# Optimization experiments

Hardware: AMD Instinct MI355X
Metric: run time of the kernel (lower is better)

The kernel has to match this reference:

```python
import jax, jax.numpy as jnp
import numpy as np

B, S, V, K = 8, 128, 32000, 32


def setup_inputs() -> dict:
    key = jax.random.key(0)
    ks = jax.random.split(key, 8)
    return {
        "neural_logit": jax.random.normal(ks[0], (B, S, V), dtype=jnp.float32),
        "optor_vals": jax.random.randint(ks[1], (B, S, K), 0, V),
        "optor_dists": jax.random.uniform(ks[2], (B, S, K), dtype=jnp.float32) * 100.0,
        "const_vals": jax.random.randint(ks[3], (B, S, K), 0, V),
        "const_dists": jax.random.uniform(ks[4], (B, S, K), dtype=jnp.float32) * 100.0,
        "prev_words": jax.random.randint(ks[5], (B, S), 0, V),
        "optor_lamda": jnp.array([0.7], dtype=jnp.float32),
        "const_lamda": jnp.array([0.7], dtype=jnp.float32),
        "optor_temp": jnp.array([10.0], dtype=jnp.float32),
        "const_temp": jnp.array([10.0], dtype=jnp.float32),
    }


def _knn_prob(vals, dists, temp, vocab):
    # kernel-density: softmax over negative distances, scatter-add into vocab ids
    b, s, k = vals.shape
    w = jax.nn.softmax(-dists / temp, axis=-1)            # [B,S,K]
    rows = jnp.arange(b * s)[:, None]                     # [BS,1]
    p = jnp.zeros((b * s, vocab), w.dtype)
    p = p.at[rows, vals.reshape(b * s, k)].add(w.reshape(b * s, k))
    return p.reshape(b, s, vocab)


def reference(neural_logit, optor_vals, optor_dists, const_vals, const_dists,
              prev_words, optor_lamda, const_lamda, optor_temp, const_temp):
    nmt_prob = jax.nn.softmax(neural_logit, axis=-1)      # [B,S,V]

    optor_knn = _knn_prob(optor_vals, optor_dists, optor_temp[0], V)
    optor_combined = optor_lamda[0] * optor_knn + (1.0 - optor_lamda[0]) * nmt_prob

    const_knn = _knn_prob(const_vals, const_dists, const_temp[0], V)
    const_combined = const_lamda[0] * const_knn + (1.0 - const_lamda[0]) * nmt_prob

    pw = prev_words                                        # [B,S]
    optor_mask = (pw <= 88) | ((pw >= 91) & (pw <= 291))
    const_mask = (pw == 89) | (pw == 90) | (pw >= 292)

    combined = (optor_combined * optor_mask[:, :, None].astype(nmt_prob.dtype)
                + const_combined * const_mask[:, :, None].astype(nmt_prob.dtype))
    return combined
```

## Files before the change

### kernel.cpp

```cpp
#include <hip/hip_runtime.h>
#include <math.h>

constexpr int Bc = 8, Sc = 128, Vc = 32000, Kc = 32;
constexpr int NROWS = Bc * Sc;
constexpr int V4 = Vc / 4;
constexpr int NT = 256;
constexpr int ITF = V4 / NT;
constexpr int TAIL = V4 - ITF * NT;
constexpr int NW = NT / 64;

typedef float vfloat4 __attribute__((ext_vector_type(4)));

__global__ __launch_bounds__(NT) void SR_knnModel_kernel(
    const float* __restrict__ logit,
    const int*   __restrict__ optor_vals,
    const float* __restrict__ optor_dists,
    const int*   __restrict__ const_vals,
    const float* __restrict__ const_dists,
    const int*   __restrict__ prev_words,
    const float* __restrict__ optor_lamda,
    const float* __restrict__ const_lamda,
    const float* __restrict__ optor_temp,
    const float* __restrict__ const_temp,
    float* __restrict__ out)
{
    const int row = blockIdx.x;
    const int t   = threadIdx.x;
    const size_t base = (size_t)row * Vc;
    const float4* __restrict__ xin  = (const float4*)(logit + base);
    float* __restrict__        orow = out + base;

    float lsum = 0.f;
#pragma unroll 4
    for (int i = 0; i < ITF; ++i) {
        const float4 v = xin[t + i * NT];
        lsum += (__expf(v.x) + __expf(v.y)) + (__expf(v.z) + __expf(v.w));
    }
    if (t < TAIL) {
        const float4 v = xin[ITF * NT + t];
        lsum += (__expf(v.x) + __expf(v.y)) + (__expf(v.z) + __expf(v.w));
    }

    const int pw = prev_words[row];
    const float ol = optor_lamda[0];
    const float cl = const_lamda[0];

#pragma unroll
    for (int off = 32; off > 0; off >>= 1)
        lsum += __shfl_xor(lsum, off);
    __shared__ float red[NW];
    if ((t & 63) == 0) red[t >> 6] = lsum;
    __syncthreads();
    float S = red[0];
#pragma unroll
    for (int w = 1; w < NW; ++w) S += red[w];

    const bool om_ = (pw <= 88) || (pw >= 91 && pw <= 291);
    const bool cm_ = (pw == 89) || (pw == 90) || (pw >= 292);
    const float omf = om_ ? 1.f : 0.f;
    const float cmf = cm_ ? 1.f : 0.f;
    const float cn = (1.f - ol) * omf + (1.f - cl) * cmf;
    const float f = cn / S;

#pragma unroll 4
    for (int i = 0; i < ITF; ++i) {
        const int idx = t + i * NT;
        const float4 v = xin[idx];
        vfloat4 o;
        o.x = __expf(v.x) * f;
        o.y = __expf(v.y) * f;
        o.z = __expf(v.z) * f;
        o.w = __expf(v.w) * f;
        __builtin_nontemporal_store(o, (vfloat4*)orow + idx);
    }
    if (t < TAIL) {
        const int idx = ITF * NT + t;
        const float4 v = xin[idx];
        vfloat4 o;
        o.x = __expf(v.x) * f;
        o.y = __expf(v.y) * f;
        o.z = __expf(v.z) * f;
        o.w = __expf(v.w) * f;
        __builtin_nontemporal_store(o, (vfloat4*)orow + idx);
    }
    __syncthreads();

    if (t < 32 || (t >= 64 && t < 96)) {
        const bool is_opt = (t < 32);
        const float scale = is_opt ? ol * omf : cl * cmf;
        if (scale != 0.f) {
            const int k = t & 31;
            const int*   vals  = is_opt ? optor_vals  : const_vals;
            const float* dists = is_opt ? optor_dists : const_dists;
            const float  temp  = is_opt ? optor_temp[0] : const_temp[0];
            const float sc = -dists[row * Kc + k] / temp;
            float mm = sc;
#pragma unroll
            for (int off = 16; off > 0; off >>= 1)
                mm = fmaxf(mm, __shfl_xor(mm, off));
            const float e = __expf(sc - mm);
            float sm = e;
#pragma unroll
            for (int off = 16; off > 0; off >>= 1)
                sm += __shfl_xor(sm, off);
            const float w = e / sm;
            atomicAdd(out + base + vals[row * Kc + k], scale * w);
        }
    }
}

extern "C" void kernel_launch(void* const* d_in, const int* in_sizes, int n_in,
                              void* d_out, int out_size, void* d_ws, size_t ws_size,
                              hipStream_t stream) {
    const float* logit       = (const float*)d_in[0];
    const int*   optor_vals  = (const int*)  d_in[1];
    const float* optor_dists = (const float*)d_in[2];
    const int*   const_vals  = (const int*)  d_in[3];
    const float* const_dists = (const float*)d_in[4];
    const int*   prev_words  = (const int*)  d_in[5];
    const float* optor_lamda = (const float*)d_in[6];
    const float* const_lamda = (const float*)d_in[7];
    const float* optor_temp  = (const float*)d_in[8];
    const float* const_temp  = (const float*)d_in[9];
    float* out = (float*)d_out;

    SR_knnModel_kernel<<<NROWS, NT, 0, stream>>>(
        logit, optor_vals, optor_dists, const_vals, const_dists, prev_words,
        optor_lamda, const_lamda, optor_temp, const_temp, out);
}
```

Measured before the change: 264.1 us.

## Split fused softmax kernel into sum, chunked scale, and scatter kernels

The single per-row kernel is replaced by three launches: one computes each row's exp-sum into workspace, a second writes the scaled probabilities with four blocks per row, and a third does the kNN scatter-add with one wave per row. The aim is more parallelism in the write pass and removing the block-wide syncs. The cost is two extra launches and a second read of the logits from memory or cache, where the fused version reread its own row.

```diff
diff --git a/kernel.cpp b/kernel.cpp
--- a/kernel.cpp
+++ b/kernel.cpp
@@ -4,15 +4,105 @@
 constexpr int Bc = 8, Sc = 128, Vc = 32000, Kc = 32;
 constexpr int NROWS = Bc * Sc;
 constexpr int V4 = Vc / 4;
-constexpr int NT = 256;
-constexpr int ITF = V4 / NT;
-constexpr int TAIL = V4 - ITF * NT;
-constexpr int NW = NT / 64;
+
+constexpr int NTA = 256;
+constexpr int ITA = V4 / NTA;
+constexpr int TLA = V4 - ITA * NTA;
+constexpr int NWA = NTA / 64;
+
+constexpr int CHUNKS = 4;
+constexpr int C4 = V4 / CHUNKS;
+constexpr int NTB = 256;
+constexpr int ITB = C4 / NTB;
+constexpr int TLB = C4 - ITB * NTB;
+
+constexpr int NTC = 256;
+constexpr int RPC = 4;
 
 typedef float vfloat4 __attribute__((ext_vector_type(4)));
 
-__global__ __launch_bounds__(NT) void SR_knnModel_kernel(
+
+__global__ __launch_bounds__(NTA) void SR_knn_sum(
     const float* __restrict__ logit,
+    float* __restrict__ ws)
+{
+    const int row = blockIdx.x;
+    const int t   = threadIdx.x;
+    const float4* __restrict__ xin = (const float4*)(logit + (size_t)row * Vc);
+
+    float lsum = 0.f;
+#pragma unroll 4
+    for (int i = 0; i < ITA; ++i) {
+        const float4 v = xin[t + i * NTA];
+        lsum += (__expf(v.x) + __expf(v.y)) + (__expf(v.z) + __expf(v.w));
+    }
+    if (t < TLA) {
+        const float4 v = xin[ITA * NTA + t];
+        lsum += (__expf(v.x) + __expf(v.y)) + (__expf(v.z) + __expf(v.w));
+    }
+
+#pragma unroll
+    for (int off = 32; off > 0; off >>= 1)
+        lsum += __shfl_xor(lsum, off);
+    __shared__ float red[NWA];
+    if ((t & 63) == 0) red[t >> 6] = lsum;
+    __syncthreads();
+    if (t == 0) {
+        float S = red[0];
+#pragma unroll
+        for (int w = 1; w < NWA; ++w) S += red[w];
+        ws[row] = S;
+    }
+}
+
+__global__ __launch_bounds__(NTB) void SR_knn_scale(
+    const float* __restrict__ logit,
+    const float* __restrict__ ws,
+    const int*   __restrict__ prev_words,
+    const float* __restrict__ optor_lamda,
+    const float* __restrict__ const_lamda,
+    float* __restrict__ out)
+{
+    const int g   = blockIdx.x;
+    const int row = g >> 2;
+    const int c   = g & (CHUNKS - 1);
+    const int t   = threadIdx.x;
+    const size_t base = (size_t)row * Vc;
+    const int off4 = c * C4;
+    const float4* __restrict__ xin  = (const float4*)(logit + base) + off4;
+    vfloat4* __restrict__      xout = (vfloat4*)(out + base) + off4;
+
+    const int pw = prev_words[row];
+    const bool om_ = (pw <= 88) || (pw >= 91 && pw <= 291);
+    const bool cm_ = (pw == 89) || (pw == 90) || (pw >= 292);
+    const float cn = (1.f - optor_lamda[0]) * (om_ ? 1.f : 0.f)
+                   + (1.f - const_lamda[0]) * (cm_ ? 1.f : 0.f);
+    const float f = cn / ws[row];
+
+#pragma unroll
+    for (int i = 0; i < ITB; ++i) {
+        const int idx = t + i * NTB;
+        const float4 v = xin[idx];
+        vfloat4 o;
+        o.x = __expf(v.x) * f;
+        o.y = __expf(v.y) * f;
+        o.z = __expf(v.z) * f;
+        o.w = __expf(v.w) * f;
+        __builtin_nontemporal_store(o, xout + idx);
+    }
+    if (t < TLB) {
+        const int idx = ITB * NTB + t;
+        const float4 v = xin[idx];
+        vfloat4 o;
+        o.x = __expf(v.x) * f;
+        o.y = __expf(v.y) * f;
+        o.z = __expf(v.z) * f;
+        o.w = __expf(v.w) * f;
+        __builtin_nontemporal_store(o, xout + idx);
+    }
+}
+
+__global__ __launch_bounds__(NTC) void SR_knn_scatter(
     const int*   __restrict__ optor_vals,
     const float* __restrict__ optor_dists,
     const int*   __restrict__ const_vals,
@@ -24,88 +114,34 @@
     const float* __restrict__ const_temp,
     float* __restrict__ out)
 {
-    const int row = blockIdx.x;
-    const int t   = threadIdx.x;
-    const size_t base = (size_t)row * Vc;
-    const float4* __restrict__ xin  = (const float4*)(logit + base);
-    float* __restrict__        orow = out + base;
-
-    float lsum = 0.f;
-#pragma unroll 4
-    for (int i = 0; i < ITF; ++i) {
-        const float4 v = xin[t + i * NT];
-        lsum += (__expf(v.x) + __expf(v.y)) + (__expf(v.z) + __expf(v.w));
-    }
-    if (t < TAIL) {
-        const float4 v = xin[ITF * NT + t];
-        lsum += (__expf(v.x) + __expf(v.y)) + (__expf(v.z) + __expf(v.w));
-    }
+    const int t    = threadIdx.x;
+    const int wave = t >> 6;
+    const int row  = blockIdx.x * RPC + wave;
+    const int lane = t & 63;
+    const bool is_opt = lane < 32;
+    const int k = lane & 31;
 
     const int pw = prev_words[row];
-    const float ol = optor_lamda[0];
-    const float cl = const_lamda[0];
-
-#pragma unroll
-    for (int off = 32; off > 0; off >>= 1)
-        lsum += __shfl_xor(lsum, off);
-    __shared__ float red[NW];
-    if ((t & 63) == 0) red[t >> 6] = lsum;
-    __syncthreads();
-    float S = red[0];
-#pragma unroll
-    for (int w = 1; w < NW; ++w) S += red[w];
-
     const bool om_ = (pw <= 88) || (pw >= 91 && pw <= 291);
     const bool cm_ = (pw == 89) || (pw == 90) || (pw >= 292);
-    const float omf = om_ ? 1.f : 0.f;
-    const float cmf = cm_ ? 1.f : 0.f;
-    const float cn = (1.f - ol) * omf + (1.f - cl) * cmf;
-    const float f = cn / S;
-
-#pragma unroll 4
-    for (int i = 0; i < ITF; ++i) {
-        const int idx = t + i * NT;
-        const float4 v = xin[idx];
-        vfloat4 o;
-        o.x = __expf(v.x) * f;
-        o.y = __expf(v.y) * f;
-        o.z = __expf(v.z) * f;
-        o.w = __expf(v.w) * f;
-        __builtin_nontemporal_store(o, (vfloat4*)orow + idx);
-    }
-    if (t < TAIL) {
-        const int idx = ITF * NT + t;
-        const float4 v = xin[idx];
-        vfloat4 o;
-        o.x = __expf(v.x) * f;
-        o.y = __expf(v.y) * f;
-        o.z = __expf(v.z) * f;
-        o.w = __expf(v.w) * f;
-        __builtin_nontemporal_store(o, (vfloat4*)orow + idx);
-    }
-    __syncthreads();
-
-    if (t < 32 || (t >= 64 && t < 96)) {
-        const bool is_opt = (t < 32);
-        const float scale = is_opt ? ol * omf : cl * cmf;
-        if (scale != 0.f) {
-            const int k = t & 31;
-            const int*   vals  = is_opt ? optor_vals  : const_vals;
-            const float* dists = is_opt ? optor_dists : const_dists;
-            const float  temp  = is_opt ? optor_temp[0] : const_temp[0];
-            const float sc = -dists[row * Kc + k] / temp;
-            float mm = sc;
+    const float scale = is_opt ? optor_lamda[0] * (om_ ? 1.f : 0.f)
+                               : const_lamda[0] * (cm_ ? 1.f : 0.f);
+    if (scale != 0.f) {
+        const int*   vals  = is_opt ? optor_vals  : const_vals;
+        const float* dists = is_opt ? optor_dists : const_dists;
+        const float  temp  = is_opt ? optor_temp[0] : const_temp[0];
+        const float sc = -dists[row * Kc + k] / temp;
+        float mm = sc;
 #pragma unroll
-            for (int off = 16; off > 0; off >>= 1)
-                mm = fmaxf(mm, __shfl_xor(mm, off));
-            const float e = __expf(sc - mm);
-            float sm = e;
+        for (int off = 16; off > 0; off >>= 1)
+            mm = fmaxf(mm, __shfl_xor(mm, off));
+        const float e = __expf(sc - mm);
+        float sm = e;
 #pragma unroll
-            for (int off = 16; off > 0; off >>= 1)
-                sm += __shfl_xor(sm, off);
-            const float w = e / sm;
-            atomicAdd(out + base + vals[row * Kc + k], scale * w);
-        }
+        for (int off = 16; off > 0; off >>= 1)
+            sm += __shfl_xor(sm, off);
+        atomicAdd(out + (size_t)row * Vc + vals[row * Kc + k],
+                  scale * (e / sm));
     }
 }
 
@@ -123,8 +159,12 @@
     const float* optor_temp  = (const float*)d_in[8];
     const float* const_temp  = (const float*)d_in[9];
     float* out = (float*)d_out;
+    float* sums = (float*)d_ws;
 
-    SR_knnModel_kernel<<<NROWS, NT, 0, stream>>>(
-        logit, optor_vals, optor_dists, const_vals, const_dists, prev_words,
+    SR_knn_sum<<<NROWS, NTA, 0, stream>>>(logit, sums);
+    SR_knn_scale<<<NROWS * CHUNKS, NTB, 0, stream>>>(
+        logit, sums, prev_words, optor_lamda, const_lamda, out);
+    SR_knn_scatter<<<NROWS / RPC, NTC, 0, stream>>>(
+        optor_vals, optor_dists, const_vals, const_dists, prev_words,
         optor_lamda, const_lamda, optor_temp, const_temp, out);
 }
```

New measurement: 269.3 us. About the same (+2.0%).

## Keep each row's exponentials in registers with 1024-thread blocks instead of rereading

Applied to the files above, without the earlier changes.

Raises the block size to 1024 threads, so each thread handles 8 float4 chunks of the row. Those chunks are held in a register array after the exponential is computed once. The second pass then scales the cached values rather than reloading logits from global memory and recomputing exp, removing one full read of the input and half the transcendental work. The cost is higher register pressure, which limits how many 1024-thread blocks can be resident per CU, and a block-wide reduction across 16 waves.

```diff
diff --git a/kernel.cpp b/kernel.cpp
--- a/kernel.cpp
+++ b/kernel.cpp
@@ -3,10 +3,9 @@
 
 constexpr int Bc = 8, Sc = 128, Vc = 32000, Kc = 32;
 constexpr int NROWS = Bc * Sc;
+constexpr int NT = 1024;
 constexpr int V4 = Vc / 4;
-constexpr int NT = 256;
-constexpr int ITF = V4 / NT;
-constexpr int TAIL = V4 - ITF * NT;
+constexpr int IT = (V4 + NT - 1) / NT;
 constexpr int NW = NT / 64;
 
 typedef float vfloat4 __attribute__((ext_vector_type(4)));
@@ -27,18 +26,21 @@
     const int row = blockIdx.x;
     const int t   = threadIdx.x;
     const size_t base = (size_t)row * Vc;
-    const float4* __restrict__ xin  = (const float4*)(logit + base);
-    float* __restrict__        orow = out + base;
+    const vfloat4* __restrict__ xin = (const vfloat4*)(logit + base);
+    vfloat4* __restrict__      xout = (vfloat4*)(out + base);
 
+    vfloat4 r[IT];
     float lsum = 0.f;
-#pragma unroll 4
-    for (int i = 0; i < ITF; ++i) {
-        const float4 v = xin[t + i * NT];
-        lsum += (__expf(v.x) + __expf(v.y)) + (__expf(v.z) + __expf(v.w));
-    }
-    if (t < TAIL) {
-        const float4 v = xin[ITF * NT + t];
-        lsum += (__expf(v.x) + __expf(v.y)) + (__expf(v.z) + __expf(v.w));
+#pragma unroll
+    for (int i = 0; i < IT; ++i) {
+        const int idx = t + i * NT;
+        if (i < IT - 1 || idx < V4) {
+            vfloat4 v = xin[idx];
+            v.x = __expf(v.x); v.y = __expf(v.y);
+            v.z = __expf(v.z); v.w = __expf(v.w);
+            r[i] = v;
+            lsum += (v.x + v.y) + (v.z + v.w);
+        }
     }
 
     const int pw = prev_words[row];
@@ -49,7 +51,8 @@
     for (int off = 32; off > 0; off >>= 1)
         lsum += __shfl_xor(lsum, off);
     __shared__ float red[NW];
-    if ((t & 63) == 0) red[t >> 6] = lsum;
+    const int wave = t >> 6;
+    if ((t & 63) == 0) red[wave] = lsum;
     __syncthreads();
     float S = red[0];
 #pragma unroll
@@ -62,26 +65,14 @@
     const float cn = (1.f - ol) * omf + (1.f - cl) * cmf;
     const float f = cn / S;
 
-#pragma unroll 4
-    for (int i = 0; i < ITF; ++i) {
+#pragma unroll
+    for (int i = 0; i < IT; ++i) {
         const int idx = t + i * NT;
-        const float4 v = xin[idx];
-        vfloat4 o;
-        o.x = __expf(v.x) * f;
-        o.y = __expf(v.y) * f;
-        o.z = __expf(v.z) * f;
-        o.w = __expf(v.w) * f;
-        __builtin_nontemporal_store(o, (vfloat4*)orow + idx);
-    }
-    if (t < TAIL) {
-        const int idx = ITF * NT + t;
-        const float4 v = xin[idx];
-        vfloat4 o;
-        o.x = __expf(v.x) * f;
-        o.y = __expf(v.y) * f;
-        o.z = __expf(v.z) * f;
-        o.w = __expf(v.w) * f;
-        __builtin_nontemporal_store(o, (vfloat4*)orow + idx);
+        if (i < IT - 1 || idx < V4) {
+            vfloat4 o = r[i];
+            o.x *= f; o.y *= f; o.z *= f; o.w *= f;
+            __builtin_nontemporal_store(o, xout + idx);
+        }
     }
     __syncthreads();
 
@@ -103,8 +94,7 @@
 #pragma unroll
             for (int off = 16; off > 0; off >>= 1)
                 sm += __shfl_xor(sm, off);
-            const float w = e / sm;
-            atomicAdd(out + base + vals[row * Kc + k], scale * w);
+            atomicAdd(out + base + vals[row * Kc + k], scale * (e / sm));
         }
     }
 }
```

Result: faster. 245.1 us (-7.2%).
